# Kernel tuning notes

Measured on AMD Instinct MI355X. Metric: run time of the kernel, lower is better.

The kernel has to match this reference:

```python
import jax, jax.numpy as jnp
import numpy as np

V, F, N = 5143, 10144, 2_000_000


def _safe_normalize(x):
    # matches GaussianAvatars safe_normalize: x / sqrt(clamp(|x|^2, min=1e-20))
    return x * jax.lax.rsqrt(jnp.clip(jnp.sum(x * x, axis=-1, keepdims=True), 1e-20, None))


def _quat_wxyz_to_rotmat(q):
    # rotation_activation (L2 normalize with eps) then wxyz->xyzw + roma unitquat_to_rotmat
    q = q / (jnp.sqrt(jnp.sum(q * q, axis=-1, keepdims=True)) + 1e-12)
    w, x, y, z = q[..., 0], q[..., 1], q[..., 2], q[..., 3]
    R = jnp.stack([
        jnp.stack([1 - 2 * (y * y + z * z), 2 * (x * y - z * w), 2 * (x * z + y * w)], axis=-1),
        jnp.stack([2 * (x * y + z * w), 1 - 2 * (x * x + z * z), 2 * (y * z - x * w)], axis=-1),
        jnp.stack([2 * (x * z - y * w), 2 * (y * z + x * w), 1 - 2 * (x * x + y * y)], axis=-1),
    ], axis=-2)
    return R  # [N,3,3]


def setup_inputs() -> dict:
    key = jax.random.key(0)
    ks = jax.random.split(key, 9)
    verts = jax.random.normal(ks[0], (V, 3), jnp.float32) * 0.1
    faces = jax.random.randint(ks[1], (F, 3), 0, V, dtype=jnp.int32)
    binding = jax.random.randint(ks[2], (N,), 0, F, dtype=jnp.int32)
    xyz = jax.random.normal(ks[3], (N, 3), jnp.float32) * 0.01
    rotation = jax.random.normal(ks[4], (N, 4), jnp.float32)
    scaling = jax.random.normal(ks[5], (N, 3), jnp.float32) - 4.0
    opacity = jax.random.normal(ks[6], (N, 1), jnp.float32)
    features_dc = jax.random.normal(ks[7], (N, 1, 3), jnp.float32)
    features_rest = jax.random.normal(ks[8], (N, 15, 3), jnp.float32) * 0.1
    return dict(verts=verts, faces=faces, binding=binding, xyz=xyz, rotation=rotation,
                scaling=scaling, opacity=opacity, features_dc=features_dc,
                features_rest=features_rest)


def reference(verts, faces, binding, xyz, rotation, scaling, opacity, features_dc, features_rest):
    # --- per-face geometry (compute_face_orientation + face_center) ---
    v0 = verts[faces[:, 0]]  # [F,3]
    v1 = verts[faces[:, 1]]
    v2 = verts[faces[:, 2]]
    face_center = (v0 + v1 + v2) / 3.0  # triangles.mean(dim=-2)
    e01 = v1 - v0
    e02 = v2 - v0
    a0 = _safe_normalize(e01)
    a1 = _safe_normalize(jnp.cross(a0, e02))
    a2 = -_safe_normalize(jnp.cross(a1, a0))
    face_orien_mat = jnp.stack([a0, a1, a2], axis=-1)  # [F,3,3], columns = axes
    s0 = jnp.sqrt(jnp.sum(e01 * e01, axis=-1, keepdims=True))
    s1 = jnp.abs(jnp.sum(a2 * e02, axis=-1, keepdims=True))
    face_scaling = 0.5 * (s0 + s1)  # [F,1]

    # --- binding-indexed gathers ---
    O_b = face_orien_mat[binding]      # [N,3,3]
    fs_b = face_scaling[binding]       # [N,1]
    fc_b = face_center[binding]        # [N,3]

    # --- gaussian position in world space ---
    xyz_out = jnp.einsum('nij,nj->ni', O_b, xyz) * fs_b + fc_b  # [N,3]

    # --- color (dc sh band 0 + opacity), scaled to 0..255 ---
    op = jax.nn.sigmoid(opacity)  # [N,1]
    color = jnp.clip((jnp.concatenate([0.5 + 0.282 * features_dc[:, 0, :], op], axis=-1)) * 255.0, 0.0, 255.0)

    # --- covariance build ---
    scales = jnp.exp(scaling) * fs_b  # [N,3]
    Q = _quat_wxyz_to_rotmat(rotation)  # [N,3,3]
    rotations = jnp.swapaxes(jnp.einsum('nij,njk->nik', O_b, Q), 1, 2)  # (O@Q)^T, [N,3,3]
    sig = rotations * scales[:, :, None]  # einsum('bij,bi->bij')
    C = jnp.einsum('nij,nik->njk', sig, sig)  # [N,3,3] = sig^T sig
    simga = jnp.stack([C[:, 0, 0], C[:, 0, 1], C[:, 0, 2], C[:, 1, 1], C[:, 1, 2], C[:, 2, 2]], axis=-1)

    return jnp.concatenate([xyz_out, color, simga], axis=-1)  # [N,13]
```

## Files before the change

kernel.cpp:

```cpp
#include <hip/hip_runtime.h>
#include <math.h>

typedef float f4 __attribute__((ext_vector_type(4)));
typedef _Float16 h8 __attribute__((ext_vector_type(8)));

struct F3 { float x, y, z; };

__device__ __forceinline__ F3 f3(float x, float y, float z) { return {x, y, z}; }
__device__ __forceinline__ F3 add(F3 a, F3 b) { return {a.x+b.x, a.y+b.y, a.z+b.z}; }
__device__ __forceinline__ F3 sub(F3 a, F3 b) { return {a.x-b.x, a.y-b.y, a.z-b.z}; }
__device__ __forceinline__ F3 mul(F3 a, float s) { return {a.x*s, a.y*s, a.z*s}; }
__device__ __forceinline__ float dot3(F3 a, F3 b) { return a.x*b.x + a.y*b.y + a.z*b.z; }
__device__ __forceinline__ F3 cross3(F3 a, F3 b) {
    return {a.y*b.z - a.z*b.y, a.z*b.x - a.x*b.z, a.x*b.y - a.y*b.x};
}
__device__ __forceinline__ F3 safe_normalize(F3 a) {
    float d = dot3(a, a);
    float inv = rsqrtf(fmaxf(d, 1e-20f));
    return mul(a, inv);
}

#define BLK 256

__global__ __launch_bounds__(BLK) void face_precompute_kernel(
    const float* __restrict__ verts, const int* __restrict__ faces,
    h8* __restrict__ tab, int F)
{
    const int f = blockIdx.x * BLK + threadIdx.x;
    if (f >= F) return;
    const int f0 = faces[3*f+0], f1 = faces[3*f+1], f2 = faces[3*f+2];
    const F3 v0 = f3(verts[3*f0], verts[3*f0+1], verts[3*f0+2]);
    const F3 v1 = f3(verts[3*f1], verts[3*f1+1], verts[3*f1+2]);
    const F3 v2 = f3(verts[3*f2], verts[3*f2+1], verts[3*f2+2]);

    const F3 fc  = mul(add(add(v0, v1), v2), (1.0f/3.0f));
    const F3 e01 = sub(v1, v0);
    const F3 e02 = sub(v2, v0);
    const F3 a0 = safe_normalize(e01);
    const F3 a1 = safe_normalize(cross3(a0, e02));
    const F3 a2 = mul(safe_normalize(cross3(a1, a0)), -1.0f);
    const float s0 = sqrtf(dot3(e01, e01));
    const float s1 = fabsf(dot3(a2, e02));
    const float fs = 0.5f * (s0 + s1);

    const float R00 = a0.x, R10 = a0.y, R20 = a0.z;
    const float R01 = a1.x, R11 = a1.y, R21 = a1.z;
    const float R02 = a2.x, R12 = a2.y, R22 = a2.z;
    float qw, qx, qy, qz;
    const float tr = R00 + R11 + R22;
    if (tr > 0.0f) {
        const float s = 0.5f / sqrtf(tr + 1.0f);
        qw = 0.25f / s;
        qx = (R21 - R12) * s;
        qy = (R02 - R20) * s;
        qz = (R10 - R01) * s;
    } else if (R00 > R11 && R00 > R22) {
        const float s = 2.0f * sqrtf(1.0f + R00 - R11 - R22);
        qw = (R21 - R12) / s;
        qx = 0.25f * s;
        qy = (R01 + R10) / s;
        qz = (R02 + R20) / s;
    } else if (R11 > R22) {
        const float s = 2.0f * sqrtf(1.0f + R11 - R00 - R22);
        qw = (R02 - R20) / s;
        qx = (R01 + R10) / s;
        qy = 0.25f * s;
        qz = (R12 + R21) / s;
    } else {
        const float s = 2.0f * sqrtf(1.0f + R22 - R00 - R11);
        qw = (R10 - R01) / s;
        qx = (R02 + R20) / s;
        qy = (R12 + R21) / s;
        qz = 0.25f * s;
    }
    const float qn = rsqrtf(fmaxf(qw*qw + qx*qx + qy*qy + qz*qz, 1e-30f));
    qw *= qn; qx *= qn; qy *= qn; qz *= qn;

    h8 rec;
    rec[0] = (_Float16)fc.x; rec[1] = (_Float16)fc.y;
    rec[2] = (_Float16)fc.z; rec[3] = (_Float16)fs;
    rec[4] = (_Float16)qw;   rec[5] = (_Float16)qx;
    rec[6] = (_Float16)qy;   rec[7] = (_Float16)qz;
    tab[f] = rec;
}

__global__ __launch_bounds__(BLK) void gauss_main_kernel(
    const h8*    __restrict__ tab,
    const int*   __restrict__ binding,
    const float* __restrict__ xyz,
    const float* __restrict__ rot,
    const float* __restrict__ scal,
    const float* __restrict__ opac,
    const float* __restrict__ fdc,
    float*       __restrict__ out,
    int N)
{
    __shared__ float sin_[3 * BLK * 3];
    __shared__ float sout[BLK * 13];

    const int tid  = threadIdx.x;
    const int base = blockIdx.x * BLK;
    const int i    = base + tid;
    const int count = min(BLK, N - base);
    const bool full = (count == BLK);

    const int b = (i < N) ? binding[i] : 0;

    h8 rec = {0,0,0,0, (_Float16)1.0f,0,0,0};
    f4 q4 = {0,0,0,1};
    float opa = 0.0f;
    if (i < N) {
        rec = tab[b];
        q4  = reinterpret_cast<const f4*>(rot)[i];
        opa = opac[i];
    }

    if (full) {
        const f4* x4 = reinterpret_cast<const f4*>(xyz  + (size_t)base * 3);
        const f4* s4 = reinterpret_cast<const f4*>(scal + (size_t)base * 3);
        const f4* d4 = reinterpret_cast<const f4*>(fdc  + (size_t)base * 3);
        f4* sv = reinterpret_cast<f4*>(sin_);
        if (tid < 192) {
            sv[      tid] = x4[tid];
            sv[192 + tid] = s4[tid];
            sv[384 + tid] = d4[tid];
        }
    }

    float px, py, pz, sc0, sc1, sc2, d0, d1, d2;
    if (full) {
        __syncthreads();
        px  = sin_[        3*tid    ]; py  = sin_[        3*tid + 1]; pz  = sin_[        3*tid + 2];
        sc0 = sin_[ 768 +  3*tid    ]; sc1 = sin_[ 768 +  3*tid + 1]; sc2 = sin_[ 768 +  3*tid + 2];
        d0  = sin_[1536 +  3*tid    ]; d1  = sin_[1536 +  3*tid + 1]; d2  = sin_[1536 +  3*tid + 2];
    } else {
        px = py = pz = sc0 = sc1 = sc2 = d0 = d1 = d2 = 0.0f;
        if (i < N) {
            px  = xyz [3*i]; py  = xyz [3*i+1]; pz  = xyz [3*i+2];
            sc0 = scal[3*i]; sc1 = scal[3*i+1]; sc2 = scal[3*i+2];
            d0  = fdc [3*i]; d1  = fdc [3*i+1]; d2  = fdc [3*i+2];
        }
    }

    if (i < N) {
        const F3 fc = f3((float)rec[0], (float)rec[1], (float)rec[2]);
        const float fs = (float)rec[3];
        const float fw = (float)rec[4], fx = (float)rec[5];
        const float fy = (float)rec[6], fz = (float)rec[7];

        const F3 p  = f3(px, py, pz);
        const F3 qv = f3(fx, fy, fz);
        const F3 tt = mul(cross3(qv, p), 2.0f);
        const F3 v  = add(add(p, mul(tt, fw)), cross3(qv, tt));
        const F3 xo = add(mul(v, fs), fc);

        const float qn = sqrtf(q4.x*q4.x + q4.y*q4.y + q4.z*q4.z + q4.w*q4.w) + 1e-12f;
        const float qi = 1.0f / qn;
        const float pw = q4.x*qi, pxq = q4.y*qi, pyq = q4.z*qi, pzq = q4.w*qi;

        const float tw = fw*pw  - fx*pxq - fy*pyq - fz*pzq;
        const float tx = fw*pxq + fx*pw  + fy*pzq - fz*pyq;
        const float ty = fw*pyq - fx*pzq + fy*pw  + fz*pxq;
        const float tz = fw*pzq + fx*pyq - fy*pxq + fz*pw;

        const F3 m0 = f3(1.0f - 2.0f*(ty*ty + tz*tz),
                         2.0f*(tx*ty + tz*tw),
                         2.0f*(tx*tz - ty*tw));
        const F3 m1 = f3(2.0f*(tx*ty - tz*tw),
                         1.0f - 2.0f*(tx*tx + tz*tz),
                         2.0f*(ty*tz + tx*tw));
        const F3 m2 = f3(2.0f*(tx*tz + ty*tw),
                         2.0f*(ty*tz - tx*tw),
                         1.0f - 2.0f*(tx*tx + ty*ty));

        const float w0 = __expf(sc0) * fs;
        const float w1 = __expf(sc1) * fs;
        const float w2 = __expf(sc2) * fs;
        const float t0s = w0*w0, t1s = w1*w1, t2s = w2*w2;

        const float C00 = t0s*m0.x*m0.x + t1s*m1.x*m1.x + t2s*m2.x*m2.x;
        const float C01 = t0s*m0.x*m0.y + t1s*m1.x*m1.y + t2s*m2.x*m2.y;
        const float C02 = t0s*m0.x*m0.z + t1s*m1.x*m1.z + t2s*m2.x*m2.z;
        const float C11 = t0s*m0.y*m0.y + t1s*m1.y*m1.y + t2s*m2.y*m2.y;
        const float C12 = t0s*m0.y*m0.z + t1s*m1.y*m1.z + t2s*m2.y*m2.z;
        const float C22 = t0s*m0.z*m0.z + t1s*m1.z*m1.z + t2s*m2.z*m2.z;

        const float sg = 1.0f / (1.0f + __expf(-opa));

        float* s = sout + tid * 13;
        s[0]  = xo.x; s[1] = xo.y; s[2] = xo.z;
        s[3]  = fminf(fmaxf((0.5f + 0.282f*d0) * 255.0f, 0.0f), 255.0f);
        s[4]  = fminf(fmaxf((0.5f + 0.282f*d1) * 255.0f, 0.0f), 255.0f);
        s[5]  = fminf(fmaxf((0.5f + 0.282f*d2) * 255.0f, 0.0f), 255.0f);
        s[6]  = fminf(fmaxf(sg * 255.0f, 0.0f), 255.0f);
        s[7]  = C00; s[8] = C01; s[9] = C02; s[10] = C11; s[11] = C12; s[12] = C22;
    }

    __syncthreads();

    const int total = count * 13;
    const size_t obase = (size_t)base * 13;
    const int n4 = total >> 2;
    const f4* sf = reinterpret_cast<const f4*>(sout);
    f4* o4 = reinterpret_cast<f4*>(out + obase);
    for (int j = tid; j < n4; j += BLK) o4[j] = sf[j];
    for (int j = (n4 << 2) + tid; j < total; j += BLK) out[obase + j] = sout[j];
}

__global__ __launch_bounds__(BLK) void gauss_fused_kernel(
    const float* __restrict__ verts, const int* __restrict__ faces,
    const int* __restrict__ binding, const float* __restrict__ xyz,
    const float* __restrict__ rot, const float* __restrict__ scal,
    const float* __restrict__ opac, const float* __restrict__ fdc,
    float* __restrict__ out, int N)
{
    const int i = blockIdx.x * BLK + threadIdx.x;
    if (i >= N) return;
    const int b = binding[i];
    const int f0 = faces[3*b+0], f1 = faces[3*b+1], f2 = faces[3*b+2];
    const F3 v0 = f3(verts[3*f0], verts[3*f0+1], verts[3*f0+2]);
    const F3 v1 = f3(verts[3*f1], verts[3*f1+1], verts[3*f1+2]);
    const F3 v2 = f3(verts[3*f2], verts[3*f2+1], verts[3*f2+2]);
    const F3 fc  = mul(add(add(v0, v1), v2), (1.0f/3.0f));
    const F3 e01 = sub(v1, v0);
    const F3 e02 = sub(v2, v0);
    const F3 a0 = safe_normalize(e01);
    const F3 a1 = safe_normalize(cross3(a0, e02));
    const float s0 = sqrtf(dot3(e01, e01));
    const F3 a2 = mul(safe_normalize(cross3(a1, a0)), -1.0f);
    const float s1 = fabsf(dot3(a2, e02));
    const float fs = 0.5f * (s0 + s1);

    const float px = xyz[3*i], py = xyz[3*i+1], pz = xyz[3*i+2];
    const float qw0 = rot[4*i], qx0 = rot[4*i+1], qy0 = rot[4*i+2], qz0 = rot[4*i+3];
    const float sc0 = scal[3*i], sc1 = scal[3*i+1], sc2 = scal[3*i+2];
    const float opa = opac[i];
    const float d0 = fdc[3*i], d1 = fdc[3*i+1], d2 = fdc[3*i+2];

    F3 xo = add(add(mul(a0, px), mul(a1, py)), mul(a2, pz));
    xo = add(mul(xo, fs), fc);

    const float qn = sqrtf(qw0*qw0 + qx0*qx0 + qy0*qy0 + qz0*qz0) + 1e-12f;
    const float qi = 1.0f / qn;
    const float w = qw0*qi, x = qx0*qi, y = qy0*qi, z = qz0*qi;
    const float Q00 = 1.0f - 2.0f*(y*y + z*z);
    const float Q01 = 2.0f*(x*y - z*w);
    const float Q02 = 2.0f*(x*z + y*w);
    const float Q10 = 2.0f*(x*y + z*w);
    const float Q11 = 1.0f - 2.0f*(x*x + z*z);
    const float Q12 = 2.0f*(y*z - x*w);
    const float Q20 = 2.0f*(x*z - y*w);
    const float Q21 = 2.0f*(y*z + x*w);
    const float Q22 = 1.0f - 2.0f*(x*x + y*y);

    const F3 m0 = add(add(mul(a0, Q00), mul(a1, Q10)), mul(a2, Q20));
    const F3 m1 = add(add(mul(a0, Q01), mul(a1, Q11)), mul(a2, Q21));
    const F3 m2 = add(add(mul(a0, Q02), mul(a1, Q12)), mul(a2, Q22));

    const float w0 = __expf(sc0) * fs;
    const float w1 = __expf(sc1) * fs;
    const float w2 = __expf(sc2) * fs;
    const float t0s = w0*w0, t1s = w1*w1, t2s = w2*w2;

    float* op = out + (size_t)i * 13;
    op[0] = xo.x; op[1] = xo.y; op[2] = xo.z;
    op[3] = fminf(fmaxf((0.5f + 0.282f*d0) * 255.0f, 0.0f), 255.0f);
    op[4] = fminf(fmaxf((0.5f + 0.282f*d1) * 255.0f, 0.0f), 255.0f);
    op[5] = fminf(fmaxf((0.5f + 0.282f*d2) * 255.0f, 0.0f), 255.0f);
    op[6] = fminf(fmaxf((1.0f/(1.0f+__expf(-opa))) * 255.0f, 0.0f), 255.0f);
    op[7]  = t0s*m0.x*m0.x + t1s*m1.x*m1.x + t2s*m2.x*m2.x;
    op[8]  = t0s*m0.x*m0.y + t1s*m1.x*m1.y + t2s*m2.x*m2.y;
    op[9]  = t0s*m0.x*m0.z + t1s*m1.x*m1.z + t2s*m2.x*m2.z;
    op[10] = t0s*m0.y*m0.y + t1s*m1.y*m1.y + t2s*m2.y*m2.y;
    op[11] = t0s*m0.y*m0.z + t1s*m1.y*m1.z + t2s*m2.y*m2.z;
    op[12] = t0s*m0.z*m0.z + t1s*m1.z*m1.z + t2s*m2.z*m2.z;
}

extern "C" void kernel_launch(void* const* d_in, const int* in_sizes, int n_in,
                              void* d_out, int out_size, void* d_ws, size_t ws_size,
                              hipStream_t stream) {
    const float* verts   = (const float*)d_in[0];
    const int*   faces   = (const int*)  d_in[1];
    const int*   binding = (const int*)  d_in[2];
    const float* xyz     = (const float*)d_in[3];
    const float* rot     = (const float*)d_in[4];
    const float* scal    = (const float*)d_in[5];
    const float* opac    = (const float*)d_in[6];
    const float* fdc     = (const float*)d_in[7];
    float* out = (float*)d_out;
    const int N = in_sizes[2];
    const int F = in_sizes[1] / 3;

    const size_t tab_bytes = (size_t)F * sizeof(h8);
    const int blocks = (N + BLK - 1) / BLK;

    if (ws_size >= tab_bytes) {
        h8* tab = (h8*)d_ws;
        const int fblocks = (F + BLK - 1) / BLK;
        face_precompute_kernel<<<fblocks, BLK, 0, stream>>>(verts, faces, tab, F);
        gauss_main_kernel<<<blocks, BLK, 0, stream>>>(
            tab, binding, xyz, rot, scal, opac, fdc, out, N);
    } else {
        gauss_fused_kernel<<<blocks, BLK, 0, stream>>>(
            verts, faces, binding, xyz, rot, scal, opac, fdc, out, N);
    }
}
```

Baseline: 43.66 us.

## Process two gaussians per thread with direct vectorized loads, dropping input LDS staging

The main kernel now handles two points per thread. It loads xyz, scaling, features_dc and opacity as float2 vectors and rotation as two float4 directly from global memory, replacing the old LDS staging pass and its barrier. The grid is halved and the output LDS buffer is doubled so the coalesced float4 store of 13 floats per point is kept. Quaternion normalization also switches from sqrt plus divide to rsqrt, which changes numerics slightly near zero. The trade-offs are higher register pressure per thread, a larger LDS footprint per block (lower occupancy), and a scalar tail path.

```diff
diff --git a/kernel.cpp b/kernel.cpp
--- a/kernel.cpp
+++ b/kernel.cpp
@@ -2,6 +2,7 @@
 #include <math.h>
 
 typedef float f4 __attribute__((ext_vector_type(4)));
+typedef float f2 __attribute__((ext_vector_type(2)));
 typedef _Float16 h8 __attribute__((ext_vector_type(8)));
 
 struct F3 { float x, y, z; };
@@ -84,7 +85,78 @@
     tab[f] = rec;
 }
 
-__global__ __launch_bounds__(BLK) void gauss_main_kernel(
+struct Out13 {
+    float o0,o1,o2,o3,o4,o5,o6,o7,o8,o9,o10,o11,o12;
+};
+
+__device__ __forceinline__ Out13 compute_point(
+    float px, float py, float pz,
+    float rw, float rx, float ry, float rz,
+    float sc0, float sc1, float sc2,
+    float opa, float d0, float d1, float d2,
+    h8 rec)
+{
+    const float fcx = (float)rec[0], fcy = (float)rec[1], fcz = (float)rec[2];
+    const float fs  = (float)rec[3];
+    const float fw  = (float)rec[4], fx = (float)rec[5];
+    const float fy  = (float)rec[6], fz = (float)rec[7];
+
+    const float ttx = 2.0f*(fy*pz - fz*py);
+    const float tty = 2.0f*(fz*px - fx*pz);
+    const float ttz = 2.0f*(fx*py - fy*px);
+    const float vx = px + fw*ttx + (fy*ttz - fz*tty);
+    const float vy = py + fw*tty + (fz*ttx - fx*ttz);
+    const float vz = pz + fw*ttz + (fx*tty - fy*ttx);
+
+    const float qd = rw*rw + rx*rx + ry*ry + rz*rz;
+    const float qi = rsqrtf(fmaxf(qd, 1e-24f));
+    const float pw = rw*qi, pxq = rx*qi, pyq = ry*qi, pzq = rz*qi;
+
+    const float tw = fw*pw  - fx*pxq - fy*pyq - fz*pzq;
+    const float tx = fw*pxq + fx*pw  + fy*pzq - fz*pyq;
+    const float ty = fw*pyq - fx*pzq + fy*pw  + fz*pxq;
+    const float tz = fw*pzq + fx*pyq - fy*pxq + fz*pw;
+
+    const float m0x = 1.0f - 2.0f*(ty*ty + tz*tz);
+    const float m0y = 2.0f*(tx*ty + tz*tw);
+    const float m0z = 2.0f*(tx*tz - ty*tw);
+    const float m1x = 2.0f*(tx*ty - tz*tw);
+    const float m1y = 1.0f - 2.0f*(tx*tx + tz*tz);
+    const float m1z = 2.0f*(ty*tz + tx*tw);
+    const float m2x = 2.0f*(tx*tz + ty*tw);
+    const float m2y = 2.0f*(ty*tz - tx*tw);
+    const float m2z = 1.0f - 2.0f*(tx*tx + ty*ty);
+
+    const float w0 = __expf(sc0) * fs;
+    const float w1 = __expf(sc1) * fs;
+    const float w2 = __expf(sc2) * fs;
+    const float t0s = w0*w0, t1s = w1*w1, t2s = w2*w2;
+
+    Out13 o;
+    o.o0 = vx*fs + fcx;
+    o.o1 = vy*fs + fcy;
+    o.o2 = vz*fs + fcz;
+    o.o3 = fminf(fmaxf((0.5f + 0.282f*d0) * 255.0f, 0.0f), 255.0f);
+    o.o4 = fminf(fmaxf((0.5f + 0.282f*d1) * 255.0f, 0.0f), 255.0f);
+    o.o5 = fminf(fmaxf((0.5f + 0.282f*d2) * 255.0f, 0.0f), 255.0f);
+    const float sg = 1.0f / (1.0f + __expf(-opa));
+    o.o6 = fminf(fmaxf(sg * 255.0f, 0.0f), 255.0f);
+    o.o7  = t0s*m0x*m0x + t1s*m1x*m1x + t2s*m2x*m2x;
+    o.o8  = t0s*m0x*m0y + t1s*m1x*m1y + t2s*m2x*m2y;
+    o.o9  = t0s*m0x*m0z + t1s*m1x*m1z + t2s*m2x*m2z;
+    o.o10 = t0s*m0y*m0y + t1s*m1y*m1y + t2s*m2y*m2y;
+    o.o11 = t0s*m0y*m0z + t1s*m1y*m1z + t2s*m2y*m2z;
+    o.o12 = t0s*m0z*m0z + t1s*m1z*m1z + t2s*m2z*m2z;
+    return o;
+}
+
+__device__ __forceinline__ void store13(float* s, const Out13& o) {
+    s[0] = o.o0;  s[1] = o.o1;  s[2]  = o.o2;  s[3]  = o.o3;
+    s[4] = o.o4;  s[5] = o.o5;  s[6]  = o.o6;  s[7]  = o.o7;
+    s[8] = o.o8;  s[9] = o.o9;  s[10] = o.o10; s[11] = o.o11; s[12] = o.o12;
+}
+
+__global__ __launch_bounds__(BLK) void gauss_main2_kernel(
     const h8*    __restrict__ tab,
     const int*   __restrict__ binding,
     const float* __restrict__ xyz,
@@ -95,111 +167,59 @@
     float*       __restrict__ out,
     int N)
 {
-    __shared__ float sin_[3 * BLK * 3];
-    __shared__ float sout[BLK * 13];
-
-    const int tid  = threadIdx.x;
-    const int base = blockIdx.x * BLK;
-    const int i    = base + tid;
-    const int count = min(BLK, N - base);
-    const bool full = (count == BLK);
-
-    const int b = (i < N) ? binding[i] : 0;
-
-    h8 rec = {0,0,0,0, (_Float16)1.0f,0,0,0};
-    f4 q4 = {0,0,0,1};
-    float opa = 0.0f;
-    if (i < N) {
-        rec = tab[b];
-        q4  = reinterpret_cast<const f4*>(rot)[i];
-        opa = opac[i];
-    }
-
-    if (full) {
-        const f4* x4 = reinterpret_cast<const f4*>(xyz  + (size_t)base * 3);
-        const f4* s4 = reinterpret_cast<const f4*>(scal + (size_t)base * 3);
-        const f4* d4 = reinterpret_cast<const f4*>(fdc  + (size_t)base * 3);
-        f4* sv = reinterpret_cast<f4*>(sin_);
-        if (tid < 192) {
-            sv[      tid] = x4[tid];
-            sv[192 + tid] = s4[tid];
-            sv[384 + tid] = d4[tid];
+    __shared__ __align__(16) float sout[2 * BLK * 13];
+
+    const int tid   = threadIdx.x;
+    const int t     = blockIdx.x * BLK + tid;
+    const int pbase = blockIdx.x * (BLK * 2);
+    const int p0    = 2 * t;
+    const int count = min(2 * BLK, N - pbase);
+
+    if (p0 + 1 < N) {
+        const int2 b2 = reinterpret_cast<const int2*>(binding)[t];
+        const f2 xa = reinterpret_cast<const f2*>(xyz )[3*t    ];
+        const f2 xb = reinterpret_cast<const f2*>(xyz )[3*t + 1];
+        const f2 xc = reinterpret_cast<const f2*>(xyz )[3*t + 2];
+        const f2 sa = reinterpret_cast<const f2*>(scal)[3*t    ];
+        const f2 sb = reinterpret_cast<const f2*>(scal)[3*t + 1];
+        const f2 scv= reinterpret_cast<const f2*>(scal)[3*t + 2];
+        const f2 da = reinterpret_cast<const f2*>(fdc )[3*t    ];
+        const f2 db = reinterpret_cast<const f2*>(fdc )[3*t + 1];
+        const f2 dc = reinterpret_cast<const f2*>(fdc )[3*t + 2];
+        const f4 qA = reinterpret_cast<const f4*>(rot )[2*t    ];
+        const f4 qB = reinterpret_cast<const f4*>(rot )[2*t + 1];
+        const f2 op2 = reinterpret_cast<const f2*>(opac)[t];
+        const h8 recA = tab[b2.x];
+        const h8 recB = tab[b2.y];
+
+        const Out13 A = compute_point(xa.x, xa.y, xb.x,
+                                      qA.x, qA.y, qA.z, qA.w,
+                                      sa.x, sa.y, sb.x,
+                                      op2.x, da.x, da.y, db.x, recA);
+        const Out13 B = compute_point(xb.y, xc.x, xc.y,
+                                      qB.x, qB.y, qB.z, qB.w,
+                                      sb.y, scv.x, scv.y,
+                                      op2.y, db.y, dc.x, dc.y, recB);
+
+        store13(sout + (size_t)(2*tid    ) * 13, A);
+        store13(sout + (size_t)(2*tid + 1) * 13, B);
+    } else {
+        for (int p = p0; p < N; ++p) {
+            const int b = binding[p];
+            const h8 rec = tab[b];
+            const Out13 o = compute_point(
+                xyz[3*p], xyz[3*p+1], xyz[3*p+2],
+                rot[4*p], rot[4*p+1], rot[4*p+2], rot[4*p+3],
+                scal[3*p], scal[3*p+1], scal[3*p+2],
+                opac[p], fdc[3*p], fdc[3*p+1], fdc[3*p+2], rec);
+            store13(sout + (size_t)(p - pbase) * 13, o);
         }
     }
 
-    float px, py, pz, sc0, sc1, sc2, d0, d1, d2;
-    if (full) {
-        __syncthreads();
-        px  = sin_[        3*tid    ]; py  = sin_[        3*tid + 1]; pz  = sin_[        3*tid + 2];
-        sc0 = sin_[ 768 +  3*tid    ]; sc1 = sin_[ 768 +  3*tid + 1]; sc2 = sin_[ 768 +  3*tid + 2];
-        d0  = sin_[1536 +  3*tid    ]; d1  = sin_[1536 +  3*tid + 1]; d2  = sin_[1536 +  3*tid + 2];
-    } else {
-        px = py = pz = sc0 = sc1 = sc2 = d0 = d1 = d2 = 0.0f;
-        if (i < N) {
-            px  = xyz [3*i]; py  = xyz [3*i+1]; pz  = xyz [3*i+2];
-            sc0 = scal[3*i]; sc1 = scal[3*i+1]; sc2 = scal[3*i+2];
-            d0  = fdc [3*i]; d1  = fdc [3*i+1]; d2  = fdc [3*i+2];
-        }
-    }
-
-    if (i < N) {
-        const F3 fc = f3((float)rec[0], (float)rec[1], (float)rec[2]);
-        const float fs = (float)rec[3];
-        const float fw = (float)rec[4], fx = (float)rec[5];
-        const float fy = (float)rec[6], fz = (float)rec[7];
-
-        const F3 p  = f3(px, py, pz);
-        const F3 qv = f3(fx, fy, fz);
-        const F3 tt = mul(cross3(qv, p), 2.0f);
-        const F3 v  = add(add(p, mul(tt, fw)), cross3(qv, tt));
-        const F3 xo = add(mul(v, fs), fc);
-
-        const float qn = sqrtf(q4.x*q4.x + q4.y*q4.y + q4.z*q4.z + q4.w*q4.w) + 1e-12f;
-        const float qi = 1.0f / qn;
-        const float pw = q4.x*qi, pxq = q4.y*qi, pyq = q4.z*qi, pzq = q4.w*qi;
-
-        const float tw = fw*pw  - fx*pxq - fy*pyq - fz*pzq;
-        const float tx = fw*pxq + fx*pw  + fy*pzq - fz*pyq;
-        const float ty = fw*pyq - fx*pzq + fy*pw  + fz*pxq;
-        const float tz = fw*pzq + fx*pyq - fy*pxq + fz*pw;
-
-        const F3 m0 = f3(1.0f - 2.0f*(ty*ty + tz*tz),
-                         2.0f*(tx*ty + tz*tw),
-                         2.0f*(tx*tz - ty*tw));
-        const F3 m1 = f3(2.0f*(tx*ty - tz*tw),
-                         1.0f - 2.0f*(tx*tx + tz*tz),
-                         2.0f*(ty*tz + tx*tw));
-        const F3 m2 = f3(2.0f*(tx*tz + ty*tw),
-                         2.0f*(ty*tz - tx*tw),
-                         1.0f - 2.0f*(tx*tx + ty*ty));
-
-        const float w0 = __expf(sc0) * fs;
-        const float w1 = __expf(sc1) * fs;
-        const float w2 = __expf(sc2) * fs;
-        const float t0s = w0*w0, t1s = w1*w1, t2s = w2*w2;
-
-        const float C00 = t0s*m0.x*m0.x + t1s*m1.x*m1.x + t2s*m2.x*m2.x;
-        const float C01 = t0s*m0.x*m0.y + t1s*m1.x*m1.y + t2s*m2.x*m2.y;
-        const float C02 = t0s*m0.x*m0.z + t1s*m1.x*m1.z + t2s*m2.x*m2.z;
-        const float C11 = t0s*m0.y*m0.y + t1s*m1.y*m1.y + t2s*m2.y*m2.y;
-        const float C12 = t0s*m0.y*m0.z + t1s*m1.y*m1.z + t2s*m2.y*m2.z;
-        const float C22 = t0s*m0.z*m0.z + t1s*m1.z*m1.z + t2s*m2.z*m2.z;
-
-        const float sg = 1.0f / (1.0f + __expf(-opa));
-
-        float* s = sout + tid * 13;
-        s[0]  = xo.x; s[1] = xo.y; s[2] = xo.z;
-        s[3]  = fminf(fmaxf((0.5f + 0.282f*d0) * 255.0f, 0.0f), 255.0f);
-        s[4]  = fminf(fmaxf((0.5f + 0.282f*d1) * 255.0f, 0.0f), 255.0f);
-        s[5]  = fminf(fmaxf((0.5f + 0.282f*d2) * 255.0f, 0.0f), 255.0f);
-        s[6]  = fminf(fmaxf(sg * 255.0f, 0.0f), 255.0f);
-        s[7]  = C00; s[8] = C01; s[9] = C02; s[10] = C11; s[11] = C12; s[12] = C22;
-    }
-
     __syncthreads();
 
     const int total = count * 13;
-    const size_t obase = (size_t)base * 13;
+    const size_t obase = (size_t)pbase * 13;
     const int n4 = total >> 2;
     const f4* sf = reinterpret_cast<const f4*>(sout);
     f4* o4 = reinterpret_cast<f4*>(out + obase);
@@ -292,15 +312,17 @@
     const int F = in_sizes[1] / 3;
 
     const size_t tab_bytes = (size_t)F * sizeof(h8);
-    const int blocks = (N + BLK - 1) / BLK;
 
     if (ws_size >= tab_bytes) {
         h8* tab = (h8*)d_ws;
         const int fblocks = (F + BLK - 1) / BLK;
         face_precompute_kernel<<<fblocks, BLK, 0, stream>>>(verts, faces, tab, F);
-        gauss_main_kernel<<<blocks, BLK, 0, stream>>>(
+        const int NT = (N + 1) / 2;
+        const int blocks = (NT + BLK - 1) / BLK;
+        gauss_main2_kernel<<<blocks, BLK, 0, stream>>>(
             tab, binding, xyz, rot, scal, opac, fdc, out, N);
     } else {
+        const int blocks = (N + BLK - 1) / BLK;
         gauss_fused_kernel<<<blocks, BLK, 0, stream>>>(
             verts, faces, binding, xyz, rot, scal, opac, fdc, out, N);
     }
```

New measurement: 43.91 us. About the same (+0.6%).
